# Kernel tuning notes

Measured on AMD Instinct MI355X. Metric: run time of the kernel, lower is better.

## Reference

```python
import jax, jax.numpy as jnp
import numpy as np

B, T, D = 64, 1024, 512
H, O = 512, 128
HALF = D // 2
ALPHA_M = 0.8


def setup_inputs() -> dict:
    key = jax.random.key(0)
    ks = jax.random.split(key, 6)
    s_in = 1.0 / np.sqrt(HALF)
    s_h = 1.0 / np.sqrt(H)
    return {
        "x": jax.random.normal(ks[0], (B, T, D), dtype=jnp.float32),
        "w1": jax.random.uniform(ks[1], (H, HALF), jnp.float32, -s_in, s_in),
        "b1": jnp.zeros((H,), jnp.float32),
        "tau1": jnp.full((H,), 3.0, jnp.float32),
        "w2": jax.random.uniform(ks[2], (H, HALF), jnp.float32, -s_in, s_in),
        "b2": jnp.zeros((H,), jnp.float32),
        "tau2": jnp.full((H,), 0.5, jnp.float32),
        "wo": jax.random.uniform(ks[3], (O, H), jnp.float32, -s_h, s_h),
        "bo": jnp.zeros((O,), jnp.float32),
    }


def reference(x, w1, b1, tau1, w2, b2, tau2, wo, bo):
    # Hoist the per-timestep branch Linears into two batched GEMMs.
    d1_in = jnp.einsum("bti,hi->tbh", x[:, :, :HALF], w1) + b1  # [T,B,H]
    d2_in = jnp.einsum("bti,hi->tbh", x[:, :, HALF:], w2) + b2  # [T,B,H]

    a1 = jax.nn.sigmoid(tau1)  # [H]
    a2 = jax.nn.sigmoid(tau2)  # [H]

    def step(carry, ins):
        d1, d2, mem = carry
        i1, i2 = ins
        d1 = a1 * d1 + (1.0 - a1) * i1
        d2 = a2 * d2 + (1.0 - a2) * i2
        mem = ALPHA_M * mem + (1.0 - ALPHA_M) * (d1 + d2)
        return (d1, d2, mem), mem

    z = jnp.zeros((x.shape[0], tau1.shape[0]), x.dtype)
    _, mems = jax.lax.scan(step, (z, z, z), (d1_in, d2_in))  # mems: [T,B,H]

    # Output projection + sigmoid, vectorized over all timesteps.
    out = jax.nn.sigmoid(jnp.einsum("tbh,oh->bto", mems, wo) + bo)  # [B,T,O]
    return out
```

## Files before the change

### kernel.cpp

```cpp
#include <hip/hip_runtime.h>


#define B_    64
#define T_    1024
#define D_    512
#define H_    512
#define O_    128
#define HALF_ 256
#define CLEN  32
#define NC    32

typedef __attribute__((ext_vector_type(4))) float        f32x4;
typedef __attribute__((ext_vector_type(2))) float        f32x2;
typedef __attribute__((ext_vector_type(8))) short        s16x8;
typedef __attribute__((ext_vector_type(4))) unsigned int u32x4;
typedef __attribute__((ext_vector_type(2))) unsigned int u32x2;

__device__ __forceinline__ unsigned short f2bf(float f) {
    unsigned u = __float_as_uint(f);
    return (unsigned short)((u + 0x7fffu + ((u >> 16) & 1u)) >> 16);
}
__device__ __forceinline__ unsigned packbf(float a, float b) {
    return (unsigned)f2bf(a) | ((unsigned)f2bf(b) << 16);
}
__device__ __forceinline__ float bflo(unsigned u) { return __uint_as_float(u << 16); }
__device__ __forceinline__ float bfu16(unsigned short u) {
    return __uint_as_float(((unsigned)u) << 16);
}
__device__ __forceinline__ float bfhi(unsigned u) { return __uint_as_float(u & 0xffff0000u); }
__device__ __forceinline__ float sigf(float x) { return 1.f / (1.f + __expf(-x)); }
__device__ __forceinline__ float guard(float dn) {
    if (fabsf(dn) < 1e-6f) dn = (dn < 0.f ? -1e-6f : 1e-6f);
    return dn;
}
__device__ __forceinline__ float pw32(float a) {
    float t = a * a; t *= t; t *= t; t *= t; t *= t; return t;
}

typedef const __attribute__((address_space(1))) unsigned int gu32;
typedef __attribute__((address_space(3))) unsigned int      lu32;
__device__ __forceinline__ void gl_lds16(const void* g, void* l) {
    __builtin_amdgcn_global_load_lds((gu32*)g, (lu32*)l, 16, 0, 0);
}

__global__ __launch_bounds__(256) void gtab_kernel(
    const float* __restrict__ tau1, const float* __restrict__ tau2,
    float* __restrict__ G1, float* __restrict__ G2)
{
    const int h = blockIdx.x * 256 + threadIdx.x;
    const float a1 = sigf(tau1[h]), a2 = sigf(tau2[h]);
    const float c1 = 0.2f * a1 / guard(0.8f - a1);
    const float c2 = 0.2f * a2 / guard(0.8f - a2);
    float pm = 1.f, p1 = 1.f, p2 = 1.f;
    for (int k = 0; k < CLEN; ++k) {
        pm *= 0.8f; p1 *= a1; p2 *= a2;
        G1[k * H_ + h] = c1 * (pm - p1);
        G2[k * H_ + h] = c2 * (pm - p2);
    }
}

__global__ __launch_bounds__(256) void wcast_kernel(
    const float* __restrict__ w1, const float* __restrict__ w2,
    const float* __restrict__ wo,
    unsigned int* __restrict__ w1b, unsigned int* __restrict__ w2b,
    unsigned int* __restrict__ wob)
{
    const float* s; unsigned int* d; int n;
    if (blockIdx.y == 0)      { s = w1; d = w1b; n = H_ * HALF_; }
    else if (blockIdx.y == 1) { s = w2; d = w2b; n = H_ * HALF_; }
    else                      { s = wo; d = wob; n = O_ * H_;    }
    int i = (blockIdx.x * 256 + threadIdx.x) * 4;
    if (i >= n) return;
    f32x4 a = *(const f32x4*)(s + i);
    u32x2 p;
    p.x = packbf(a.x, a.y);
    p.y = packbf(a.z, a.w);
    *(u32x2*)(d + i / 2) = p;
}

__global__ __launch_bounds__(256) void cast_kernel(const float* __restrict__ x,
                                                   unsigned int* __restrict__ xb) {
    size_t i = ((size_t)blockIdx.x * 256 + threadIdx.x) * 8;
    f32x4 a = *(const f32x4*)(x + i);
    f32x4 b = *(const f32x4*)(x + i + 4);
    u32x4 p;
    p.x = packbf(a.x, a.y); p.y = packbf(a.z, a.w);
    p.z = packbf(b.x, b.y); p.w = packbf(b.z, b.w);
    *(u32x4*)(xb + i / 2) = p;
}

__global__ __launch_bounds__(512, 4) void gemm1f_kernel(
    const unsigned short* __restrict__ xb,
    const unsigned short* __restrict__ w1b, const unsigned short* __restrict__ w2b,
    const float* __restrict__ b1, const float* __restrict__ tau1,
    const float* __restrict__ b2, const float* __restrict__ tau2,
    unsigned int* __restrict__ mems,
    float* __restrict__ Sd1, float* __restrict__ Sd2, float* __restrict__ Sm)
{
    __shared__ short smem[32768];
    short* d1L = smem;
    short* d2L = smem + 16384;

    const int nt = blockIdx.x;
    const int mt = blockIdx.y;
    const int b  = mt >> 3;
    const int t0 = (mt & 7) << 7;

    const int tid = threadIdx.x, l = tid & 63, wv = tid >> 6;
    const int ln = l & 15, qd = l >> 4;
    const int wm = (wv & 1) << 6;
    const int wn = (wv >> 1) << 5;

    const unsigned short* abase  = xb + (size_t)(mt * 128) * D_;
    const unsigned short* w1base = w1b + (size_t)(nt * 128) * HALF_;
    const unsigned short* w2base = w2b + (size_t)(nt * 128) * HALF_;

    const int kb = wv >> 1;
    const int rr = ((wv & 1) << 6) + l;
    const int dst = wv * 512 + l * 8;

    f32x4 acc0[4][2] = {};
    f32x4 acc1[4][2] = {};

    {
        short* base = smem;
        gl_lds16(abase  + (size_t)rr * D_    + kb * 8,         base + dst);
        gl_lds16(abase  + (size_t)rr * D_    + HALF_ + kb * 8, base + 4096  + dst);
        gl_lds16(w1base + (size_t)rr * HALF_ + kb * 8,         base + 8192  + dst);
        gl_lds16(w2base + (size_t)rr * HALF_ + kb * 8,         base + 12288 + dst);
    }
    asm volatile("s_waitcnt vmcnt(0)" ::: "memory");
    __builtin_amdgcn_s_barrier();

    int cur = 0;
    for (int t = 0; t < 8; ++t) {
        if (t < 7) {
            short* nb = smem + (cur ^ 1) * 16384;
            int kt = (t + 1) * 32;
            gl_lds16(abase  + (size_t)rr * D_    + kt + kb * 8,         nb + dst);
            gl_lds16(abase  + (size_t)rr * D_    + HALF_ + kt + kb * 8, nb + 4096  + dst);
            gl_lds16(w1base + (size_t)rr * HALF_ + kt + kb * 8,         nb + 8192  + dst);
            gl_lds16(w2base + (size_t)rr * HALF_ + kt + kb * 8,         nb + 12288 + dst);
        }
        {
            short* base = smem + cur * 16384;
            s16x8 af[4], bfv[2];
            #pragma unroll
            for (int i = 0; i < 4; ++i) {
                int r = wm + i * 16 + ln;
                af[i] = *(const s16x8*)&base[qd * 1024 + r * 8];
            }
            #pragma unroll
            for (int j = 0; j < 2; ++j) {
                int r = wn + j * 16 + ln;
                bfv[j] = *(const s16x8*)&base[8192 + qd * 1024 + r * 8];
            }
            #pragma unroll
            for (int i = 0; i < 4; ++i)
                #pragma unroll
                for (int j = 0; j < 2; ++j)
                    acc0[i][j] = __builtin_amdgcn_mfma_f32_16x16x32_bf16(
                        af[i], bfv[j], acc0[i][j], 0, 0, 0);
            #pragma unroll
            for (int i = 0; i < 4; ++i) {
                int r = wm + i * 16 + ln;
                af[i] = *(const s16x8*)&base[4096 + qd * 1024 + r * 8];
            }
            #pragma unroll
            for (int j = 0; j < 2; ++j) {
                int r = wn + j * 16 + ln;
                bfv[j] = *(const s16x8*)&base[12288 + qd * 1024 + r * 8];
            }
            #pragma unroll
            for (int i = 0; i < 4; ++i)
                #pragma unroll
                for (int j = 0; j < 2; ++j)
                    acc1[i][j] = __builtin_amdgcn_mfma_f32_16x16x32_bf16(
                        af[i], bfv[j], acc1[i][j], 0, 0, 0);
        }
        asm volatile("s_waitcnt vmcnt(0)" ::: "memory");
        __builtin_amdgcn_s_barrier();
        cur ^= 1;
    }

    #pragma unroll
    for (int i = 0; i < 4; ++i)
        #pragma unroll
        for (int j = 0; j < 2; ++j)
            #pragma unroll
            for (int r = 0; r < 4; ++r) {
                int t  = wm + i * 16 + qd * 4 + r;
                int hc = (wn + j * 16 + ln) ^ ((t & 12) << 2);
                d1L[t * 128 + hc] = (short)f2bf(acc0[i][j][r]);
                d2L[t * 128 + hc] = (short)f2bf(acc1[i][j][r]);
            }
    __syncthreads();

    const int cl = tid >> 7;
    const int h  = tid & 127;
    const int hg = nt * 128 + h;
    const int cg = ((mt & 7) << 2) + cl;

    const float a1 = sigf(tau1[hg]);
    const float a2 = sigf(tau2[hg]);
    const float o1 = 1.f - a1, o2 = 1.f - a2;
    const float bb1 = b1[hg], bb2 = b2[hg];

    float d1 = 0.f, d2 = 0.f, m = 0.f;
    unsigned short* msh = (unsigned short*)mems;
    const size_t mrow = (size_t)(b * T_ + t0 + cl * CLEN) * H_ + hg;

    #pragma unroll 8
    for (int k = 0; k < CLEN; ++k) {
        int t  = cl * CLEN + k;
        int hc = h ^ ((t & 12) << 2);
        float i1 = bfu16((unsigned short)d1L[t * 128 + hc]) + bb1;
        float i2 = bfu16((unsigned short)d2L[t * 128 + hc]) + bb2;
        d1 = a1 * d1 + o1 * i1;
        d2 = a2 * d2 + o2 * i2;
        m  = 0.8f * m + 0.2f * (d1 + d2);
        msh[mrow + (size_t)k * H_] = f2bf(m);
    }

    const size_t si = (size_t)(cg * B_ + b) * H_ + hg;
    Sd1[si] = d1;
    Sd2[si] = d2;
    Sm[si]  = m;
}

__global__ __launch_bounds__(128) void scanB_kernel(
    const float* __restrict__ Sd1, const float* __restrict__ Sd2,
    const float* __restrict__ Sm,
    const float* __restrict__ tau1, const float* __restrict__ tau2,
    float* __restrict__ D1, float* __restrict__ D2, float* __restrict__ DM)
{
    const int g = blockIdx.x * 128 + threadIdx.x;
    const int h2 = g & 255, b = g >> 8, h0 = h2 << 1;

    const float a1a = sigf(tau1[h0]), a1b = sigf(tau1[h0 + 1]);
    const float a2a = sigf(tau2[h0]), a2b = sigf(tau2[h0 + 1]);
    const float amL = pw32(0.8f);
    const float a1La = pw32(a1a), a1Lb = pw32(a1b);
    const float a2La = pw32(a2a), a2Lb = pw32(a2b);

    const float c1a = 0.2f * a1a / guard(0.8f - a1a);
    const float c1b = 0.2f * a1b / guard(0.8f - a1b);
    const float c2a = 0.2f * a2a / guard(0.8f - a2a);
    const float c2b = 0.2f * a2b / guard(0.8f - a2b);

    const float g1La = c1a * (amL - a1La), g1Lb = c1b * (amL - a1Lb);
    const float g2La = c2a * (amL - a2La), g2Lb = c2b * (amL - a2Lb);

    float D1a = 0.f, D1b = 0.f, D2a = 0.f, D2b = 0.f, Ma = 0.f, Mb = 0.f;
    for (int c = 0; c < NC; ++c) {
        const size_t si = (size_t)(c * B_ + b) * H_ + h0;
        f32x2 v;
        v.x = D1a; v.y = D1b; *(f32x2*)&D1[si] = v;
        v.x = D2a; v.y = D2b; *(f32x2*)&D2[si] = v;
        v.x = Ma;  v.y = Mb;  *(f32x2*)&DM[si] = v;
        f32x2 s1 = *(const f32x2*)&Sd1[si];
        f32x2 s2 = *(const f32x2*)&Sd2[si];
        f32x2 sm = *(const f32x2*)&Sm[si];
        float nMa = amL * Ma + D1a * g1La + D2a * g2La + sm.x;
        float nMb = amL * Mb + D1b * g1Lb + D2b * g2Lb + sm.y;
        D1a = a1La * D1a + s1.x;  D1b = a1Lb * D1b + s1.y;
        D2a = a2La * D2a + s2.x;  D2b = a2Lb * D2b + s2.y;
        Ma = nMa;  Mb = nMb;
    }
}

__global__ __launch_bounds__(512, 4) void gemm2f_kernel(
    const unsigned short* __restrict__ mems, const unsigned short* __restrict__ wob,
    const float* __restrict__ bo,
    const float* __restrict__ G1, const float* __restrict__ G2,
    const float* __restrict__ D1, const float* __restrict__ D2,
    const float* __restrict__ DM, float* __restrict__ out)
{
    __shared__ short As[128 * 64];
    __shared__ short Bs[128 * 64];
    __shared__ float PMl[CLEN];

    const int mt = blockIdx.x;
    const int b = mt >> 3, c0 = (mt & 7) << 2;
    const int tid = threadIdx.x, l = tid & 63, wv = tid >> 6;
    const int ln = l & 15, qd = l >> 4;
    const int wm = (wv & 1) << 6;
    const int wn = (wv >> 1) << 5;

    if (tid < CLEN) {
        float pm = 1.f;
        for (int k = 0; k <= tid; ++k) pm *= 0.8f;
        PMl[tid] = pm;
    }
    __syncthreads();

    f32x4 acc[4][2] = {};
    const unsigned short* abase = mems + (size_t)(mt * 128) * H_;

    for (int kt = 0; kt < H_; kt += 64) {
        #pragma unroll
        for (int i = 0; i < 2; ++i) {
            int ch = wv * 2 + i;
            int r  = ch * 8 + (l >> 3);
            int kbl = (l & 7) ^ (r & 7);
            gl_lds16(wob + (size_t)r * H_ + kt + kbl * 8, &Bs[ch * 512 + l * 8]);
        }
        #pragma unroll
        for (int i = 0; i < 2; ++i) {
            int gi = i * 512 + tid;
            int r = gi >> 3, kbp = gi & 7, kbl = kbp ^ (r & 7);
            int h0 = kt + kbl * 8;
            int k = r & 31, c = c0 + (r >> 5);
            size_t dbase = (size_t)(c * B_ + b) * H_ + h0;
            f32x4 d1a = *(const f32x4*)&D1[dbase], d1b = *(const f32x4*)&D1[dbase + 4];
            f32x4 d2a = *(const f32x4*)&D2[dbase], d2b = *(const f32x4*)&D2[dbase + 4];
            f32x4 dma = *(const f32x4*)&DM[dbase], dmb = *(const f32x4*)&DM[dbase + 4];
            f32x4 g1a = *(const f32x4*)&G1[k * H_ + h0], g1b = *(const f32x4*)&G1[k * H_ + h0 + 4];
            f32x4 g2a = *(const f32x4*)&G2[k * H_ + h0], g2b = *(const f32x4*)&G2[k * H_ + h0 + 4];
            float pm = PMl[k];
            u32x4 mv = *(const u32x4*)(abase + (size_t)r * H_ + h0);
            float v0 = bflo(mv.x) + d1a.x * g1a.x + d2a.x * g2a.x + dma.x * pm;
            float v1 = bfhi(mv.x) + d1a.y * g1a.y + d2a.y * g2a.y + dma.y * pm;
            float v2 = bflo(mv.y) + d1a.z * g1a.z + d2a.z * g2a.z + dma.z * pm;
            float v3 = bfhi(mv.y) + d1a.w * g1a.w + d2a.w * g2a.w + dma.w * pm;
            float v4 = bflo(mv.z) + d1b.x * g1b.x + d2b.x * g2b.x + dmb.x * pm;
            float v5 = bfhi(mv.z) + d1b.y * g1b.y + d2b.y * g2b.y + dmb.y * pm;
            float v6 = bflo(mv.w) + d1b.z * g1b.z + d2b.z * g2b.z + dmb.z * pm;
            float v7 = bfhi(mv.w) + d1b.w * g1b.w + d2b.w * g2b.w + dmb.w * pm;
            u32x4 p;
            p.x = packbf(v0, v1); p.y = packbf(v2, v3);
            p.z = packbf(v4, v5); p.w = packbf(v6, v7);
            *(u32x4*)&As[r * 64 + kbp * 8] = p;
        }
        __syncthreads();
        #pragma unroll
        for (int ks = 0; ks < 64; ks += 32) {
            s16x8 af[4], bfv[2];
            #pragma unroll
            for (int i = 0; i < 4; ++i) {
                int r = wm + i * 16 + ln;
                int kbp = ((ks >> 3) + qd) ^ (r & 7);
                af[i] = *(const s16x8*)&As[r * 64 + kbp * 8];
            }
            #pragma unroll
            for (int j = 0; j < 2; ++j) {
                int r = wn + j * 16 + ln;
                int kbp = ((ks >> 3) + qd) ^ (r & 7);
                bfv[j] = *(const s16x8*)&Bs[r * 64 + kbp * 8];
            }
            #pragma unroll
            for (int i = 0; i < 4; ++i)
                #pragma unroll
                for (int j = 0; j < 2; ++j)
                    acc[i][j] = __builtin_amdgcn_mfma_f32_16x16x32_bf16(
                        af[i], bfv[j], acc[i][j], 0, 0, 0);
        }
        __syncthreads();
    }

    float bov[2];
    #pragma unroll
    for (int j = 0; j < 2; ++j) bov[j] = bo[wn + j * 16 + ln];

    float* orow = out + (size_t)(mt * 128 + wm + qd * 4) * O_ + wn + ln;
    #pragma unroll
    for (int i = 0; i < 4; ++i)
        #pragma unroll
        for (int j = 0; j < 2; ++j)
            #pragma unroll
            for (int r = 0; r < 4; ++r) {
                float v = acc[i][j][r] + bov[j];
                orow[(size_t)(i * 16 + r) * O_ + j * 16] = 1.f / (1.f + __expf(-v));
            }
}

extern "C" void kernel_launch(void* const* d_in, const int* in_sizes, int n_in,
                              void* d_out, int out_size, void* d_ws, size_t ws_size,
                              hipStream_t stream) {
    const float* x    = (const float*)d_in[0];
    const float* w1   = (const float*)d_in[1];
    const float* b1   = (const float*)d_in[2];
    const float* tau1 = (const float*)d_in[3];
    const float* w2   = (const float*)d_in[4];
    const float* b2   = (const float*)d_in[5];
    const float* tau2 = (const float*)d_in[6];
    const float* wo   = (const float*)d_in[7];
    const float* bo   = (const float*)d_in[8];
    float* out = (float*)d_out;

    char* w = (char*)d_ws;
    unsigned short* xb   = (unsigned short*)(w);
    unsigned int*   mems = (unsigned int*)(w + (size_t)64 * 1024 * 1024);
    float* Sd1 = (float*)(w + (size_t)128 * 1024 * 1024);
    float* Sd2 = Sd1 + (1u << 20);
    float* Sm  = Sd1 + (2u << 20);
    float* D1  = Sd1 + (3u << 20);
    float* D2  = Sd1 + (4u << 20);
    float* DM  = Sd1 + (5u << 20);
    float* G1  = Sd1 + (6u << 20);
    float* G2  = G1 + CLEN * H_;
    unsigned short* w1b = (unsigned short*)(G2 + CLEN * H_);
    unsigned short* w2b = w1b + (size_t)H_ * HALF_;
    unsigned short* wob = w2b + (size_t)H_ * HALF_;

    gtab_kernel<<<dim3(2), 256, 0, stream>>>(tau1, tau2, G1, G2);
    wcast_kernel<<<dim3(128, 3), 256, 0, stream>>>(w1, w2, wo,
                                                   (unsigned int*)w1b,
                                                   (unsigned int*)w2b,
                                                   (unsigned int*)wob);
    cast_kernel<<<dim3(16384), 256, 0, stream>>>(x, (unsigned int*)xb);
    gemm1f_kernel<<<dim3(4, 512), 512, 0, stream>>>(xb, w1b, w2b, b1, tau1, b2, tau2,
                                                    mems, Sd1, Sd2, Sm);
    scanB_kernel<<<dim3(128), 128, 0, stream>>>(Sd1, Sd2, Sm, tau1, tau2, D1, D2, DM);
    gemm2f_kernel<<<dim3(512), 512, 0, stream>>>((const unsigned short*)mems, wob, bo,
                                                 G1, G2, D1, D2, DM, out);
}
```

Baseline: 377.3 us.

## Load GEMM weight fragments straight to registers and widen K-step with swizzled LDS

The input-projection GEMM prologue now stages only the x tiles through LDS, using an XOR-swizzled row layout and a K-step of 64 instead of 32. This halves the number of barrier-synchronised iterations. The w1/w2 B-operand fragments are loaded directly from global memory into registers, with each next tile prefetched after the current half's MFMAs. This removes the LDS traffic and bank conflicts for the weights but adds register pressure and exposes global load latency behind the per-iteration vmcnt(0) wait.

```diff
diff --git a/kernel.cpp b/kernel.cpp
--- a/kernel.cpp
+++ b/kernel.cpp
@@ -115,72 +115,85 @@
     const unsigned short* w1base = w1b + (size_t)(nt * 128) * HALF_;
     const unsigned short* w2base = w2b + (size_t)(nt * 128) * HALF_;
 
-    const int kb = wv >> 1;
-    const int rr = ((wv & 1) << 6) + l;
-    const int dst = wv * 512 + l * 8;
-
     f32x4 acc0[4][2] = {};
     f32x4 acc1[4][2] = {};
-
-    {
-        short* base = smem;
-        gl_lds16(abase  + (size_t)rr * D_    + kb * 8,         base + dst);
-        gl_lds16(abase  + (size_t)rr * D_    + HALF_ + kb * 8, base + 4096  + dst);
-        gl_lds16(w1base + (size_t)rr * HALF_ + kb * 8,         base + 8192  + dst);
-        gl_lds16(w2base + (size_t)rr * HALF_ + kb * 8,         base + 12288 + dst);
-    }
+    s16x8 bv1[2][2], bv2[2][2];
+
+    auto stageA = [&](int kt, int ph) {
+        short* p = smem + ph * 16384;
+        #pragma unroll
+        for (int i = 0; i < 2; ++i) {
+            int ch = wv * 2 + i;
+            int r  = ch * 8 + (l >> 3);
+            int kbl = (l & 7) ^ (r & 7);
+            gl_lds16(abase + (size_t)r * D_ + kt + kbl * 8,         p + ch * 512 + l * 8);
+            gl_lds16(abase + (size_t)r * D_ + HALF_ + kt + kbl * 8, p + 8192 + ch * 512 + l * 8);
+        }
+    };
+    auto loadB1 = [&](int kt) {
+        #pragma unroll
+        for (int j = 0; j < 2; ++j)
+            #pragma unroll
+            for (int s = 0; s < 2; ++s)
+                bv1[j][s] = *(const s16x8*)(w1base +
+                    (size_t)(wn + j * 16 + ln) * HALF_ + kt + s * 32 + qd * 8);
+    };
+    auto loadB2 = [&](int kt) {
+        #pragma unroll
+        for (int j = 0; j < 2; ++j)
+            #pragma unroll
+            for (int s = 0; s < 2; ++s)
+                bv2[j][s] = *(const s16x8*)(w2base +
+                    (size_t)(wn + j * 16 + ln) * HALF_ + kt + s * 32 + qd * 8);
+    };
+
+    stageA(0, 0);
+    loadB1(0);
+    loadB2(0);
     asm volatile("s_waitcnt vmcnt(0)" ::: "memory");
     __builtin_amdgcn_s_barrier();
 
-    int cur = 0;
-    for (int t = 0; t < 8; ++t) {
-        if (t < 7) {
-            short* nb = smem + (cur ^ 1) * 16384;
-            int kt = (t + 1) * 32;
-            gl_lds16(abase  + (size_t)rr * D_    + kt + kb * 8,         nb + dst);
-            gl_lds16(abase  + (size_t)rr * D_    + HALF_ + kt + kb * 8, nb + 4096  + dst);
-            gl_lds16(w1base + (size_t)rr * HALF_ + kt + kb * 8,         nb + 8192  + dst);
-            gl_lds16(w2base + (size_t)rr * HALF_ + kt + kb * 8,         nb + 12288 + dst);
-        }
-        {
-            short* base = smem + cur * 16384;
-            s16x8 af[4], bfv[2];
+    #pragma unroll
+    for (int t = 0; t < 4; ++t) {
+        const int ph = t & 1;
+        short* base = smem + ph * 16384;
+        if (t < 3) stageA((t + 1) * 64, ph ^ 1);
+        #pragma unroll
+        for (int s = 0; s < 2; ++s) {
+            s16x8 af[4];
             #pragma unroll
             for (int i = 0; i < 4; ++i) {
                 int r = wm + i * 16 + ln;
-                af[i] = *(const s16x8*)&base[qd * 1024 + r * 8];
-            }
-            #pragma unroll
-            for (int j = 0; j < 2; ++j) {
-                int r = wn + j * 16 + ln;
-                bfv[j] = *(const s16x8*)&base[8192 + qd * 1024 + r * 8];
+                int kbp = ((s << 2) + qd) ^ (r & 7);
+                af[i] = *(const s16x8*)&base[r * 64 + kbp * 8];
             }
             #pragma unroll
             for (int i = 0; i < 4; ++i)
                 #pragma unroll
                 for (int j = 0; j < 2; ++j)
                     acc0[i][j] = __builtin_amdgcn_mfma_f32_16x16x32_bf16(
-                        af[i], bfv[j], acc0[i][j], 0, 0, 0);
+                        af[i], bv1[j][s], acc0[i][j], 0, 0, 0);
+        }
+        if (t < 3) loadB1((t + 1) * 64);
+        #pragma unroll
+        for (int s = 0; s < 2; ++s) {
+            s16x8 af[4];
             #pragma unroll
             for (int i = 0; i < 4; ++i) {
                 int r = wm + i * 16 + ln;
-                af[i] = *(const s16x8*)&base[4096 + qd * 1024 + r * 8];
-            }
-            #pragma unroll
-            for (int j = 0; j < 2; ++j) {
-                int r = wn + j * 16 + ln;
-                bfv[j] = *(const s16x8*)&base[12288 + qd * 1024 + r * 8];
+                int kbp = ((s << 2) + qd) ^ (r & 7);
+                af[i] = *(const s16x8*)&base[8192 + r * 64 + kbp * 8];
             }
             #pragma unroll
             for (int i = 0; i < 4; ++i)
                 #pragma unroll
                 for (int j = 0; j < 2; ++j)
                     acc1[i][j] = __builtin_amdgcn_mfma_f32_16x16x32_bf16(
-                        af[i], bfv[j], acc1[i][j], 0, 0, 0);
-        }
+                        af[i], bv2[j][s], acc1[i][j], 0, 0, 0);
+        }
+        if (t < 3) loadB2((t + 1) * 64);
         asm volatile("s_waitcnt vmcnt(0)" ::: "memory");
         __builtin_amdgcn_s_barrier();
-        cur ^= 1;
     }
 
     #pragma unroll
```

Measured after the change: 369.7 us. 2.0% less time.
